# Kernel optimization log

Measured on AMD Instinct MI355X. Metric: run time of the kernel, lower is better.

Reference implementation:

```python
import jax, jax.numpy as jnp
import numpy as np

NUM_HEADS = 4
HEAD_DIM = 32
QUERY_DIM = 256
KEY_DIM = 128
INNER = NUM_HEADS * HEAD_DIM  # 128


def setup_inputs() -> dict:
    key = jax.random.key(0)
    ks = jax.random.split(key, 8)
    B, T, D, H, W = 2, 4, QUERY_DIM, 40, 40
    C, Hm, Wm = KEY_DIM, 40, 40
    query = jax.random.normal(ks[0], (B, T, D, H, W), dtype=jnp.float32)
    k_in = jax.random.normal(ks[1], (B, T, C, Hm, Wm), dtype=jnp.float32)
    v_in = jax.random.normal(ks[2], (B, T, C, Hm, Wm), dtype=jnp.float32)
    # Linear weights stored as (in, out); torch nn.Linear init ~ U(-1/sqrt(in), 1/sqrt(in))
    def lin(k, fan_in, fan_out):
        bound = 1.0 / np.sqrt(fan_in)
        return jax.random.uniform(k, (fan_in, fan_out), minval=-bound, maxval=bound, dtype=jnp.float32)
    Wq = lin(ks[3], QUERY_DIM, INNER)
    Wk = lin(ks[4], KEY_DIM, INNER)
    Wv = lin(ks[5], KEY_DIM, INNER)
    Wo = lin(ks[6], INNER, QUERY_DIM)
    bo = jax.random.uniform(ks[7], (QUERY_DIM,), minval=-1.0 / np.sqrt(INNER), maxval=1.0 / np.sqrt(INNER), dtype=jnp.float32)
    return {"query": query, "key": k_in, "value": v_in,
            "Wq": Wq, "Wk": Wk, "Wv": Wv, "Wo": Wo, "bo": bo}


def reference(query, key, value, Wq, Wk, Wv, Wo, bo):
    B, T, D, H, W = query.shape
    _, _, C, Hm, Wm = key.shape
    scale = HEAD_DIM ** (-0.5)
    # b t d h w -> b t (h w) d
    q = query.reshape(B, T, D, H * W).transpose(0, 1, 3, 2)
    k = key.reshape(B, T, C, Hm * Wm).transpose(0, 1, 3, 2)
    v = value.reshape(B, T, C, Hm * Wm).transpose(0, 1, 3, 2)
    # projections then split heads: b t n (h d) -> b t h n d
    def heads(x):
        Bn, Tn, N, _ = x.shape
        return x.reshape(Bn, Tn, N, NUM_HEADS, HEAD_DIM).transpose(0, 1, 3, 2, 4)
    Q = heads(q @ Wq)
    K = heads(k @ Wk)
    V = heads(v @ Wv)
    scores = jnp.einsum('bthqd,bthkd->bthqk', Q, K) * scale
    probs = jax.nn.softmax(scores, axis=-1)
    out = jnp.einsum('bthqk,bthkd->bthqd', probs, V)
    # b t h n d -> b t n (h d)
    out = out.transpose(0, 1, 3, 2, 4).reshape(B, T, H * W, INNER)
    fused = out @ Wo + bo
    # b t (h w) d -> b t d h w
    return fused.transpose(0, 1, 3, 2).reshape(B, T, D, H, W)
```

## Files before the change

kernel.cpp:

```cpp
#include <hip/hip_runtime.h>

#define NTOK 1600
#define BT_TOTAL 8
#define INNER 128
#define HD 32
#define NH 4
#define QDIM 256

typedef short short8 __attribute__((ext_vector_type(8)));
typedef short short4v __attribute__((ext_vector_type(4)));
typedef float f32x2 __attribute__((ext_vector_type(2)));
typedef float f32x4 __attribute__((ext_vector_type(4)));
typedef float f32x16 __attribute__((ext_vector_type(16)));
typedef unsigned uint2v __attribute__((ext_vector_type(2)));

__device__ inline short f2b(float x) {
  union { float f; unsigned u; } v; v.f = x;
  unsigned r = (v.u + 0x7FFF + ((v.u >> 16) & 1)) >> 16;
  return (short)r;
}
__device__ inline unsigned cvtpk(float a, float b) {
  unsigned r;
  asm("v_cvt_pk_bf16_f32 %0, %1, %2" : "=v"(r) : "v"(a), "v"(b));
  return r;
}
__device__ inline void pswap(unsigned &a, unsigned &b) {
  uint2v r = __builtin_amdgcn_permlane32_swap(a, b, false, false);
  a = r[0]; b = r[1];
}
__device__ inline short8 ldsfrag(const short* p) {
  short4v a = *(const short4v*)p;
  short4v b = *(const short4v*)(p + 4);
  short8 r;
  r[0] = a[0]; r[1] = a[1]; r[2] = a[2]; r[3] = a[3];
  r[4] = b[0]; r[5] = b[1]; r[6] = b[2]; r[7] = b[3];
  return r;
}
__device__ inline short8 mk8(unsigned a, unsigned b, unsigned c, unsigned d) {
  union { unsigned u[4]; short8 v; } t;
  t.u[0] = a; t.u[1] = b; t.u[2] = c; t.u[3] = d;
  return t.v;
}

__global__ __launch_bounds__(256) void proj_fused(
    const float* __restrict__ query, const float* __restrict__ Wq,
    const float* __restrict__ key, const float* __restrict__ Wk,
    const float* __restrict__ value, const float* __restrict__ Wv,
    short* __restrict__ Qbf, short* __restrict__ Kbf,
    short* __restrict__ Vbf) {
  const int n0 = blockIdx.x * 64;
  const int which = blockIdx.y;
  const int bt = blockIdx.z;
  const int t = threadIdx.x;
  const int lane = t & 63, w = t >> 6;
  const int quad = lane >> 4, n16 = lane & 15;

  const float* X; const float* Wt; short* Y; int nchunk; float scl;
  if (which == 0) {
    X = query; Wt = Wq; Y = Qbf; nchunk = 8;
    scl = 0.17677669529663687f * 1.4426950408889634f;
  } else if (which == 1) {
    X = key; Wt = Wk; Y = Kbf; nchunk = 4; scl = 1.0f;
  } else {
    X = value; Wt = Wv; Y = Vbf; nchunk = 4; scl = 1.0f;
  }
  const float* Xb = X + (size_t)bt * (nchunk * 32) * NTOK;

  __shared__ short Xs[64 * 36];
  __shared__ short Ws[128 * 36];

  f32x4 acc[8];
#pragma unroll
  for (int i = 0; i < 8; ++i) acc[i] = (f32x4){0.f, 0.f, 0.f, 0.f};

  const int iw = t & 127, g = t >> 7;

  float xf0[4], xf1[4], wf0[8], wf1[8];
  auto loadX = [&](int cd) {
#pragma unroll
    for (int dp = 0; dp < 4; ++dp) {
      int dl = w * 8 + dp * 2;
      xf0[dp] = Xb[(size_t)(cd + dl) * NTOK + n0 + lane];
      xf1[dp] = Xb[(size_t)(cd + dl + 1) * NTOK + n0 + lane];
    }
  };
  auto loadW = [&](int cd) {
#pragma unroll
    for (int dp = 0; dp < 8; ++dp) {
      int dl = g * 16 + dp * 2;
      wf0[dp] = Wt[(size_t)(cd + dl) * INNER + iw];
      wf1[dp] = Wt[(size_t)(cd + dl + 1) * INNER + iw];
    }
  };
  loadX(0); loadW(0);

  for (int c = 0; c < nchunk; ++c) {
#pragma unroll
    for (int dp = 0; dp < 4; ++dp)
      *(unsigned*)&Xs[lane * 36 + w * 8 + dp * 2] = cvtpk(xf0[dp], xf1[dp]);
#pragma unroll
    for (int dp = 0; dp < 8; ++dp)
      *(unsigned*)&Ws[iw * 36 + g * 16 + dp * 2] = cvtpk(wf0[dp], wf1[dp]);
    __syncthreads();
    if (c + 1 < nchunk) { loadX((c + 1) * 32); loadW((c + 1) * 32); }
    if (which != 2) {
      short8 a[4], b[2];
#pragma unroll
      for (int tg = 0; tg < 4; ++tg)
        a[tg] = ldsfrag(&Xs[(tg * 16 + n16) * 36 + quad * 8]);
#pragma unroll
      for (int cg = 0; cg < 2; ++cg)
        b[cg] = ldsfrag(&Ws[(w * 32 + cg * 16 + n16) * 36 + quad * 8]);
#pragma unroll
      for (int tg = 0; tg < 4; ++tg)
#pragma unroll
        for (int cg = 0; cg < 2; ++cg)
          acc[tg * 2 + cg] = __builtin_amdgcn_mfma_f32_16x16x32_bf16(
              a[tg], b[cg], acc[tg * 2 + cg], 0, 0, 0);
    } else {
      short8 a[2], b[4];
#pragma unroll
      for (int ig = 0; ig < 2; ++ig)
        a[ig] = ldsfrag(&Ws[(w * 32 + ig * 16 + n16) * 36 + quad * 8]);
#pragma unroll
      for (int tg = 0; tg < 4; ++tg)
        b[tg] = ldsfrag(&Xs[(tg * 16 + n16) * 36 + quad * 8]);
#pragma unroll
      for (int ig = 0; ig < 2; ++ig)
#pragma unroll
        for (int tg = 0; tg < 4; ++tg)
          acc[ig * 4 + tg] = __builtin_amdgcn_mfma_f32_16x16x32_bf16(
              a[ig], b[tg], acc[ig * 4 + tg], 0, 0, 0);
    }
    __syncthreads();
  }

  if (which != 2) {
    short* Yb = Y + ((size_t)bt * NH + w) * NTOK * HD;
#pragma unroll
    for (int tg = 0; tg < 4; ++tg)
#pragma unroll
      for (int cg = 0; cg < 2; ++cg) {
        f32x4 a = acc[tg * 2 + cg];
#pragma unroll
        for (int r = 0; r < 4; ++r) {
          int tok = n0 + tg * 16 + quad * 4 + r;
          Yb[(size_t)tok * HD + cg * 16 + n16] = f2b(a[r] * scl);
        }
      }
  } else {
#pragma unroll
    for (int ig = 0; ig < 2; ++ig)
#pragma unroll
      for (int tg = 0; tg < 4; ++tg) {
        f32x4 a = acc[ig * 4 + tg];
#pragma unroll
        for (int r = 0; r < 4; ++r) {
          int irow = w * 32 + ig * 16 + quad * 4 + r;
          Y[((size_t)bt * INNER + irow) * NTOK + n0 + tg * 16 + n16] =
              f2b(a[r]);
        }
      }
  }
}

__global__ __launch_bounds__(256, 3) void attn_mfma(
    const short* __restrict__ Qb, const short* __restrict__ Kb,
    const short* __restrict__ Vb, short* __restrict__ Obf) {
  const int id = blockIdx.x;
  const int qt = id >> 5;
  const int pair = id & 31;
  const int bt = pair >> 2, h = pair & 3;
  const int wave = threadIdx.x >> 6, lane = threadIdx.x & 63;
  const int lh = lane >> 5, q32 = lane & 31;
  const int q0 = qt * 64;
  const size_t btok = ((size_t)bt * NH + h) * NTOK;
  const size_t bd = ((size_t)bt * NH + h) * HD;

  __shared__ float Cb[2][2][17][64];

  const short* QpA = &Qb[(btok + q0 + q32) * HD + lh * 8];
  const short* QpB = QpA + 32 * HD;
  const short8 bqA0 = *(const short8*)(QpA);
  const short8 bqA1 = *(const short8*)(QpA + 16);
  const short8 bqB0 = *(const short8*)(QpB);
  const short8 bqB1 = *(const short8*)(QpB + 16);

  const int kstart = wave * 416 - (wave == 3 ? 32 : 0);
  const int nch = 13 - (wave >> 1);
  const short* Kp = &Kb[(btok + kstart + q32) * HD + lh * 8];
  const short* Vp = &Vb[(bd + q32) * NTOK + kstart + lh * 8];

  const f32x16 zero16 = {0.f, 0.f, 0.f, 0.f, 0.f, 0.f, 0.f, 0.f,
                         0.f, 0.f, 0.f, 0.f, 0.f, 0.f, 0.f, 0.f};
  f32x16 oA = zero16, oB = zero16;
  f32x2 lsA = {0.f, 0.f}, lsB = {0.f, 0.f};

  auto softmax_pack = [&](const f32x16& sv, f32x2& ls2, short8& pb0,
                          short8& pb1) {
    unsigned Pd[8];
#pragma unroll
    for (int g = 0; g < 4; ++g) {
      float e0 = __builtin_amdgcn_exp2f(sv[4 * g + 0]);
      float e1 = __builtin_amdgcn_exp2f(sv[4 * g + 1]);
      float e2 = __builtin_amdgcn_exp2f(sv[4 * g + 2]);
      float e3 = __builtin_amdgcn_exp2f(sv[4 * g + 3]);
      ls2 += (f32x2){e0, e1};
      ls2 += (f32x2){e2, e3};
      Pd[2 * g + 0] = cvtpk(e0, e1);
      Pd[2 * g + 1] = cvtpk(e2, e3);
    }
    pswap(Pd[0], Pd[2]);
    pswap(Pd[1], Pd[3]);
    pswap(Pd[4], Pd[6]);
    pswap(Pd[5], Pd[7]);
    pb0 = mk8(Pd[0], Pd[1], Pd[2], Pd[3]);
    pb1 = mk8(Pd[4], Pd[5], Pd[6], Pd[7]);
  };

  short8 ak0 = *(const short8*)(Kp);
  short8 ak1 = *(const short8*)(Kp + 16);
  short8 av0 = *(const short8*)(Vp);
  short8 av1 = *(const short8*)(Vp + 16);

  for (int i = 0; i < nch; ++i) {
    const size_t kn = (i + 1 < nch) ? (size_t)(i + 1) * 32 : 0;
    short8 nk0 = *(const short8*)(Kp + kn * HD);
    short8 nk1 = *(const short8*)(Kp + kn * HD + 16);
    short8 nv0 = *(const short8*)(Vp + kn);
    short8 nv1 = *(const short8*)(Vp + kn + 16);

    f32x16 sA = __builtin_amdgcn_mfma_f32_32x32x16_bf16(ak0, bqA0, zero16,
                                                        0, 0, 0);
    sA = __builtin_amdgcn_mfma_f32_32x32x16_bf16(ak1, bqA1, sA, 0, 0, 0);
    f32x16 sB = __builtin_amdgcn_mfma_f32_32x32x16_bf16(ak0, bqB0, zero16,
                                                        0, 0, 0);
    sB = __builtin_amdgcn_mfma_f32_32x32x16_bf16(ak1, bqB1, sB, 0, 0, 0);

    short8 pbA0, pbA1, pbB0, pbB1;
    softmax_pack(sA, lsA, pbA0, pbA1);
    softmax_pack(sB, lsB, pbB0, pbB1);

    oA = __builtin_amdgcn_mfma_f32_32x32x16_bf16(av0, pbA0, oA, 0, 0, 0);
    oA = __builtin_amdgcn_mfma_f32_32x32x16_bf16(av1, pbA1, oA, 0, 0, 0);
    oB = __builtin_amdgcn_mfma_f32_32x32x16_bf16(av0, pbB0, oB, 0, 0, 0);
    oB = __builtin_amdgcn_mfma_f32_32x32x16_bf16(av1, pbB1, oB, 0, 0, 0);

    ak0 = nk0; ak1 = nk1; av0 = nv0; av1 = nv1;
  }

  float lsumA = lsA[0] + lsA[1];
  lsumA += __shfl_xor(lsumA, 32);
  float lsumB = lsB[0] + lsB[1];
  lsumB += __shfl_xor(lsumB, 32);

  auto dump = [&](int tl, int sidx, const f32x16& o, float ls) {
#pragma unroll
    for (int r = 0; r < 16; ++r) Cb[tl][sidx][r][lane] = o[r];
    Cb[tl][sidx][16][lane] = ls;
  };
  auto accum = [&](int tl, int sidx, f32x16& o, float& ls) {
#pragma unroll
    for (int r = 0; r < 16; ++r) o[r] += Cb[tl][sidx][r][lane];
    ls += Cb[tl][sidx][16][lane];
  };
  if (wave == 1) { dump(0, 0, oA, lsumA); dump(1, 0, oB, lsumB); }
  if (wave == 3) { dump(0, 1, oA, lsumA); dump(1, 1, oB, lsumB); }
  __syncthreads();
  if (wave == 0) { accum(0, 0, oA, lsumA); accum(1, 0, oB, lsumB); }
  if (wave == 2) { accum(0, 1, oA, lsumA); accum(1, 1, oB, lsumB); }
  __syncthreads();
  if (wave == 2) { dump(0, 0, oA, lsumA); dump(1, 0, oB, lsumB); }
  __syncthreads();
  if (wave == 0) {
    accum(0, 0, oA, lsumA);
    accum(1, 0, oB, lsumB);
    const float invA = 1.f / lsumA;
    short* OpA =
        &Obf[((size_t)bt * NTOK + q0 + q32) * INNER + h * HD + lh * 4];
#pragma unroll
    for (int g = 0; g < 4; ++g) {
      unsigned d0 = cvtpk(oA[4 * g + 0] * invA, oA[4 * g + 1] * invA);
      unsigned d1 = cvtpk(oA[4 * g + 2] * invA, oA[4 * g + 3] * invA);
      *(uint2*)&OpA[8 * g] = make_uint2(d0, d1);
    }
    const float invB = 1.f / lsumB;
    short* OpB =
        &Obf[((size_t)bt * NTOK + q0 + 32 + q32) * INNER + h * HD + lh * 4];
#pragma unroll
    for (int g = 0; g < 4; ++g) {
      unsigned d0 = cvtpk(oB[4 * g + 0] * invB, oB[4 * g + 1] * invB);
      unsigned d1 = cvtpk(oB[4 * g + 2] * invB, oB[4 * g + 3] * invB);
      *(uint2*)&OpB[8 * g] = make_uint2(d0, d1);
    }
  }
}

__global__ __launch_bounds__(256) void oproj_mfma(
    const short* __restrict__ Obf, const float* __restrict__ Wo,
    const float* __restrict__ bo, float* __restrict__ out) {
  const int tok0 = blockIdx.x * 64, d0 = blockIdx.y * 64;
  const int bt = blockIdx.z;
  const int t = threadIdx.x, lane = t & 63, w = t >> 6;
  const int quad = lane >> 4, n16 = lane & 15;
  __shared__ short Wos[64 * 36];
  f32x4 acc[4];
#pragma unroll
  for (int i = 0; i < 4; ++i) acc[i] = (f32x4){0.f, 0.f, 0.f, 0.f};
  const int tok = tok0 + w * 16 + n16;

  float wf0[4], wf1[4];
  short8 bfr;
  auto loadWo = [&](int c) {
#pragma unroll
    for (int dp = 0; dp < 4; ++dp) {
      int il = w * 8 + dp * 2;
      wf0[dp] = Wo[(size_t)(c * 32 + il) * QDIM + d0 + lane];
      wf1[dp] = Wo[(size_t)(c * 32 + il + 1) * QDIM + d0 + lane];
    }
  };
  auto loadB = [&](int c) {
    bfr = *(const short8*)&Obf[((size_t)bt * NTOK + tok) * INNER + c * 32 +
                               quad * 8];
  };
  loadWo(0); loadB(0);

  for (int c = 0; c < 4; ++c) {
#pragma unroll
    for (int dp = 0; dp < 4; ++dp)
      *(unsigned*)&Wos[lane * 36 + w * 8 + dp * 2] = cvtpk(wf0[dp], wf1[dp]);
    __syncthreads();
    short8 b0 = bfr;
    if (c < 3) { loadWo(c + 1); loadB(c + 1); }
#pragma unroll
    for (int ag = 0; ag < 4; ++ag) {
      short8 a = ldsfrag(&Wos[(ag * 16 + n16) * 36 + quad * 8]);
      acc[ag] = __builtin_amdgcn_mfma_f32_16x16x32_bf16(a, b0, acc[ag], 0, 0, 0);
    }
    __syncthreads();
  }

#pragma unroll
  for (int ag = 0; ag < 4; ++ag) {
    f32x4 a = acc[ag];
#pragma unroll
    for (int r = 0; r < 4; ++r) {
      int dout = d0 + ag * 16 + quad * 4 + r;
      out[((size_t)bt * QDIM + dout) * NTOK + tok] = a[r] + bo[dout];
    }
  }
}

extern "C" void kernel_launch(void* const* d_in, const int* in_sizes, int n_in,
                              void* d_out, int out_size, void* d_ws,
                              size_t ws_size, hipStream_t stream) {
  const float* query = (const float*)d_in[0];
  const float* key = (const float*)d_in[1];
  const float* value = (const float*)d_in[2];
  const float* Wq = (const float*)d_in[3];
  const float* Wk = (const float*)d_in[4];
  const float* Wv = (const float*)d_in[5];
  const float* Wo = (const float*)d_in[6];
  const float* bo = (const float*)d_in[7];
  float* out = (float*)d_out;

  const size_t arr = (size_t)BT_TOTAL * INNER * NTOK;
  short* Qbf = (short*)d_ws;
  short* Kbf = Qbf + arr;
  short* Vbf = Kbf + arr;
  short* Obf = Vbf + arr;

  proj_fused<<<dim3(25, 3, BT_TOTAL), 256, 0, stream>>>(
      query, Wq, key, Wk, value, Wv, Qbf, Kbf, Vbf);
  attn_mfma<<<dim3(800), 256, 0, stream>>>(Qbf, Kbf, Vbf, Obf);
  oproj_mfma<<<dim3(25, 4, BT_TOTAL), 256, 0, stream>>>(Obf, Wo, bo, out);
}
```

Baseline: 120.3 us.

## Fuse three kernels into one persistent kernel with grid barriers

Replaces the three separate launches (projection, attention, output projection) with a single persistent kernel of 512 blocks that pull work items from atomic counters and separate the phases with software grid barriers. This is meant to remove launch gaps and tail effects between kernels. The cost is an extra memset, atomic contention, and barrier spin time. Occupancy drops because launch bounds go from 3 to 2 blocks per SM for attention. The design also assumes all 512 blocks are co-resident; if they are not, the grid barrier deadlocks.

Result: slower. 300.9 us (+150.0%).

```diff
diff --git a/kernel.cpp b/kernel.cpp
--- a/kernel.cpp
+++ b/kernel.cpp
@@ -6,6 +6,8 @@
 #define HD 32
 #define NH 4
 #define QDIM 256
+
+#define NBLK 512
 
 typedef short short8 __attribute__((ext_vector_type(8)));
 typedef short short4v __attribute__((ext_vector_type(4)));
@@ -42,15 +44,30 @@
   return t.v;
 }
 
-__global__ __launch_bounds__(256) void proj_fused(
-    const float* __restrict__ query, const float* __restrict__ Wq,
-    const float* __restrict__ key, const float* __restrict__ Wk,
-    const float* __restrict__ value, const float* __restrict__ Wv,
-    short* __restrict__ Qbf, short* __restrict__ Kbf,
-    short* __restrict__ Vbf) {
-  const int n0 = blockIdx.x * 64;
-  const int which = blockIdx.y;
-  const int bt = blockIdx.z;
+__device__ inline void grid_barrier(unsigned* bar, unsigned target) {
+  __syncthreads();
+  if (threadIdx.x == 0) {
+    __threadfence();
+    __hip_atomic_fetch_add(bar, 1u, __ATOMIC_RELAXED,
+                           __HIP_MEMORY_SCOPE_AGENT);
+    while (__hip_atomic_load(bar, __ATOMIC_RELAXED,
+                             __HIP_MEMORY_SCOPE_AGENT) < target) {
+      __builtin_amdgcn_s_sleep(2);
+    }
+    __threadfence();
+  }
+  __syncthreads();
+}
+
+__device__ inline void proj_item(
+    int item, char* smem, const float* __restrict__ query,
+    const float* __restrict__ Wq, const float* __restrict__ key,
+    const float* __restrict__ Wk, const float* __restrict__ value,
+    const float* __restrict__ Wv, short* __restrict__ Qbf,
+    short* __restrict__ Kbf, short* __restrict__ Vbf) {
+  const int n0 = (item % 25) * 64;
+  const int which = (item / 25) % 3;
+  const int bt = item / 75;
   const int t = threadIdx.x;
   const int lane = t & 63, w = t >> 6;
   const int quad = lane >> 4, n16 = lane & 15;
@@ -66,8 +83,8 @@
   }
   const float* Xb = X + (size_t)bt * (nchunk * 32) * NTOK;
 
-  __shared__ short Xs[64 * 36];
-  __shared__ short Ws[128 * 36];
+  short* Xs = (short*)smem;
+  short* Ws = Xs + 64 * 36;
 
   f32x4 acc[8];
 #pragma unroll
@@ -164,12 +181,13 @@
   }
 }
 
-__global__ __launch_bounds__(256, 3) void attn_mfma(
-    const short* __restrict__ Qb, const short* __restrict__ Kb,
-    const short* __restrict__ Vb, short* __restrict__ Obf) {
-  const int id = blockIdx.x;
-  const int qt = id >> 5;
-  const int pair = id & 31;
+__device__ inline void attn_item(int item, char* smem,
+                                 const short* __restrict__ Qb,
+                                 const short* __restrict__ Kb,
+                                 const short* __restrict__ Vb,
+                                 short* __restrict__ Obf) {
+  const int qt = item >> 5;
+  const int pair = item & 31;
   const int bt = pair >> 2, h = pair & 3;
   const int wave = threadIdx.x >> 6, lane = threadIdx.x & 63;
   const int lh = lane >> 5, q32 = lane & 31;
@@ -177,7 +195,7 @@
   const size_t btok = ((size_t)bt * NH + h) * NTOK;
   const size_t bd = ((size_t)bt * NH + h) * HD;
 
-  __shared__ float Cb[2][2][17][64];
+  float (*Cb)[2][17][64] = (float (*)[2][17][64])smem;
 
   const short* QpA = &Qb[(btok + q0 + q32) * HD + lh * 8];
   const short* QpB = QpA + 32 * HD;
@@ -296,14 +314,17 @@
   }
 }
 
-__global__ __launch_bounds__(256) void oproj_mfma(
-    const short* __restrict__ Obf, const float* __restrict__ Wo,
-    const float* __restrict__ bo, float* __restrict__ out) {
-  const int tok0 = blockIdx.x * 64, d0 = blockIdx.y * 64;
-  const int bt = blockIdx.z;
+__device__ inline void oproj_item(int item, char* smem,
+                                  const short* __restrict__ Obf,
+                                  const float* __restrict__ Wo,
+                                  const float* __restrict__ bo,
+                                  float* __restrict__ out) {
+  const int tok0 = (item % 25) * 64;
+  const int d0 = ((item / 25) % 4) * 64;
+  const int bt = item / 100;
   const int t = threadIdx.x, lane = t & 63, w = t >> 6;
   const int quad = lane >> 4, n16 = lane & 15;
-  __shared__ short Wos[64 * 36];
+  short* Wos = (short*)smem;
   f32x4 acc[4];
 #pragma unroll
   for (int i = 0; i < 4; ++i) acc[i] = (f32x4){0.f, 0.f, 0.f, 0.f};
@@ -335,7 +356,8 @@
 #pragma unroll
     for (int ag = 0; ag < 4; ++ag) {
       short8 a = ldsfrag(&Wos[(ag * 16 + n16) * 36 + quad * 8]);
-      acc[ag] = __builtin_amdgcn_mfma_f32_16x16x32_bf16(a, b0, acc[ag], 0, 0, 0);
+      acc[ag] =
+          __builtin_amdgcn_mfma_f32_16x16x32_bf16(a, b0, acc[ag], 0, 0, 0);
     }
     __syncthreads();
   }
@@ -348,6 +370,47 @@
       int dout = d0 + ag * 16 + quad * 4 + r;
       out[((size_t)bt * QDIM + dout) * NTOK + tok] = a[r] + bo[dout];
     }
+  }
+}
+
+__global__ __launch_bounds__(256, 2) void fused_all(
+    const float* __restrict__ query, const float* __restrict__ Wq,
+    const float* __restrict__ key, const float* __restrict__ Wk,
+    const float* __restrict__ value, const float* __restrict__ Wv,
+    const float* __restrict__ Wo, const float* __restrict__ bo,
+    short* __restrict__ Qbf, short* __restrict__ Kbf,
+    short* __restrict__ Vbf, short* __restrict__ Obf,
+    float* __restrict__ out, unsigned* __restrict__ ctrs) {
+  __shared__ __align__(16) char smem[17408];
+  __shared__ int item_s;
+
+  for (;;) {
+    __syncthreads();
+    if (threadIdx.x == 0) item_s = (int)atomicAdd(&ctrs[1], 1u);
+    __syncthreads();
+    const int item = item_s;
+    if (item >= 600) break;
+    proj_item(item, smem, query, Wq, key, Wk, value, Wv, Qbf, Kbf, Vbf);
+  }
+  grid_barrier(&ctrs[0], NBLK);
+
+  for (;;) {
+    __syncthreads();
+    if (threadIdx.x == 0) item_s = (int)atomicAdd(&ctrs[2], 1u);
+    __syncthreads();
+    const int item = item_s;
+    if (item >= 800) break;
+    attn_item(item, smem, Qbf, Kbf, Vbf, Obf);
+  }
+  grid_barrier(&ctrs[0], 2 * NBLK);
+
+  for (;;) {
+    __syncthreads();
+    if (threadIdx.x == 0) item_s = (int)atomicAdd(&ctrs[3], 1u);
+    __syncthreads();
+    const int item = item_s;
+    if (item >= 800) break;
+    oproj_item(item, smem, Obf, Wo, bo, out);
   }
 }
 
@@ -369,9 +432,9 @@
   short* Kbf = Qbf + arr;
   short* Vbf = Kbf + arr;
   short* Obf = Vbf + arr;
-
-  proj_fused<<<dim3(25, 3, BT_TOTAL), 256, 0, stream>>>(
-      query, Wq, key, Wk, value, Wv, Qbf, Kbf, Vbf);
-  attn_mfma<<<dim3(800), 256, 0, stream>>>(Qbf, Kbf, Vbf, Obf);
-  oproj_mfma<<<dim3(25, 4, BT_TOTAL), 256, 0, stream>>>(Obf, Wo, bo, out);
-}
+  unsigned* ctrs = (unsigned*)(Obf + arr);
+
+  hipMemsetAsync(ctrs, 0, 4 * sizeof(unsigned), stream);
+  fused_all<<<dim3(NBLK), dim3(256), 0, stream>>>(
+      query, Wq, key, Wk, value, Wv, Wo, bo, Qbf, Kbf, Vbf, Obf, out, ctrs);
+}
```

## Process five 32-query tiles per attention block to reuse K/V loads

Applied to the files above, without the earlier changes.

Each attention block now handles 160 queries (five 32-row tiles) instead of 64, so every K/V chunk loaded into registers feeds five score/PV MFMA pairs rather than two. The grid shrinks from 800 to 320 blocks and launch bounds drop to 2 blocks per SM to make room for the extra accumulator registers. The cross-wave LDS reduction grows to cover five tiles. The aim is to cut redundant K/V global traffic per query, at the cost of higher register pressure, lower occupancy and fewer blocks to spread across CUs.

Result: slower. 123.1 us (+2.3%).

```diff
diff --git a/kernel.cpp b/kernel.cpp
--- a/kernel.cpp
+++ b/kernel.cpp
@@ -164,27 +164,28 @@
   }
 }
 
-__global__ __launch_bounds__(256, 3) void attn_mfma(
+__global__ __launch_bounds__(256, 2) void attn_mfma(
     const short* __restrict__ Qb, const short* __restrict__ Kb,
     const short* __restrict__ Vb, short* __restrict__ Obf) {
   const int id = blockIdx.x;
-  const int qt = id >> 5;
+  const int qg = id >> 5;
   const int pair = id & 31;
   const int bt = pair >> 2, h = pair & 3;
   const int wave = threadIdx.x >> 6, lane = threadIdx.x & 63;
   const int lh = lane >> 5, q32 = lane & 31;
-  const int q0 = qt * 64;
+  const int q0 = qg * 160;
   const size_t btok = ((size_t)bt * NH + h) * NTOK;
   const size_t bd = ((size_t)bt * NH + h) * HD;
 
-  __shared__ float Cb[2][2][17][64];
-
-  const short* QpA = &Qb[(btok + q0 + q32) * HD + lh * 8];
-  const short* QpB = QpA + 32 * HD;
-  const short8 bqA0 = *(const short8*)(QpA);
-  const short8 bqA1 = *(const short8*)(QpA + 16);
-  const short8 bqB0 = *(const short8*)(QpB);
-  const short8 bqB1 = *(const short8*)(QpB + 16);
+  __shared__ float Cb[5][2][17][64];
+
+  short8 bq0[5], bq1[5];
+#pragma unroll
+  for (int tl = 0; tl < 5; ++tl) {
+    const short* Qp = &Qb[(btok + q0 + tl * 32 + q32) * HD + lh * 8];
+    bq0[tl] = *(const short8*)(Qp);
+    bq1[tl] = *(const short8*)(Qp + 16);
+  }
 
   const int kstart = wave * 416 - (wave == 3 ? 32 : 0);
   const int nch = 13 - (wave >> 1);
@@ -193,8 +194,10 @@
 
   const f32x16 zero16 = {0.f, 0.f, 0.f, 0.f, 0.f, 0.f, 0.f, 0.f,
                          0.f, 0.f, 0.f, 0.f, 0.f, 0.f, 0.f, 0.f};
-  f32x16 oA = zero16, oB = zero16;
-  f32x2 lsA = {0.f, 0.f}, lsB = {0.f, 0.f};
+  f32x16 o[5];
+  f32x2 ls[5];
+#pragma unroll
+  for (int tl = 0; tl < 5; ++tl) { o[tl] = zero16; ls[tl] = (f32x2){0.f, 0.f}; }
 
   auto softmax_pack = [&](const f32x16& sv, f32x2& ls2, short8& pb0,
                           short8& pb1) {
@@ -230,68 +233,73 @@
     short8 nv0 = *(const short8*)(Vp + kn);
     short8 nv1 = *(const short8*)(Vp + kn + 16);
 
-    f32x16 sA = __builtin_amdgcn_mfma_f32_32x32x16_bf16(ak0, bqA0, zero16,
-                                                        0, 0, 0);
-    sA = __builtin_amdgcn_mfma_f32_32x32x16_bf16(ak1, bqA1, sA, 0, 0, 0);
-    f32x16 sB = __builtin_amdgcn_mfma_f32_32x32x16_bf16(ak0, bqB0, zero16,
-                                                        0, 0, 0);
-    sB = __builtin_amdgcn_mfma_f32_32x32x16_bf16(ak1, bqB1, sB, 0, 0, 0);
-
-    short8 pbA0, pbA1, pbB0, pbB1;
-    softmax_pack(sA, lsA, pbA0, pbA1);
-    softmax_pack(sB, lsB, pbB0, pbB1);
-
-    oA = __builtin_amdgcn_mfma_f32_32x32x16_bf16(av0, pbA0, oA, 0, 0, 0);
-    oA = __builtin_amdgcn_mfma_f32_32x32x16_bf16(av1, pbA1, oA, 0, 0, 0);
-    oB = __builtin_amdgcn_mfma_f32_32x32x16_bf16(av0, pbB0, oB, 0, 0, 0);
-    oB = __builtin_amdgcn_mfma_f32_32x32x16_bf16(av1, pbB1, oB, 0, 0, 0);
+#pragma unroll
+    for (int tl = 0; tl < 5; ++tl) {
+      f32x16 s = __builtin_amdgcn_mfma_f32_32x32x16_bf16(ak0, bq0[tl], zero16,
+                                                         0, 0, 0);
+      s = __builtin_amdgcn_mfma_f32_32x32x16_bf16(ak1, bq1[tl], s, 0, 0, 0);
+      short8 pb0, pb1;
+      softmax_pack(s, ls[tl], pb0, pb1);
+      o[tl] = __builtin_amdgcn_mfma_f32_32x32x16_bf16(av0, pb0, o[tl], 0, 0, 0);
+      o[tl] = __builtin_amdgcn_mfma_f32_32x32x16_bf16(av1, pb1, o[tl], 0, 0, 0);
+    }
 
     ak0 = nk0; ak1 = nk1; av0 = nv0; av1 = nv1;
   }
 
-  float lsumA = lsA[0] + lsA[1];
-  lsumA += __shfl_xor(lsumA, 32);
-  float lsumB = lsB[0] + lsB[1];
-  lsumB += __shfl_xor(lsumB, 32);
-
-  auto dump = [&](int tl, int sidx, const f32x16& o, float ls) {
-#pragma unroll
-    for (int r = 0; r < 16; ++r) Cb[tl][sidx][r][lane] = o[r];
-    Cb[tl][sidx][16][lane] = ls;
-  };
-  auto accum = [&](int tl, int sidx, f32x16& o, float& ls) {
-#pragma unroll
-    for (int r = 0; r < 16; ++r) o[r] += Cb[tl][sidx][r][lane];
-    ls += Cb[tl][sidx][16][lane];
-  };
-  if (wave == 1) { dump(0, 0, oA, lsumA); dump(1, 0, oB, lsumB); }
-  if (wave == 3) { dump(0, 1, oA, lsumA); dump(1, 1, oB, lsumB); }
-  __syncthreads();
-  if (wave == 0) { accum(0, 0, oA, lsumA); accum(1, 0, oB, lsumB); }
-  if (wave == 2) { accum(0, 1, oA, lsumA); accum(1, 1, oB, lsumB); }
-  __syncthreads();
-  if (wave == 2) { dump(0, 0, oA, lsumA); dump(1, 0, oB, lsumB); }
+  float lsum[5];
+#pragma unroll
+  for (int tl = 0; tl < 5; ++tl) {
+    lsum[tl] = ls[tl][0] + ls[tl][1];
+    lsum[tl] += __shfl_xor(lsum[tl], 32);
+  }
+
+  auto dump = [&](int tl, int sidx) {
+#pragma unroll
+    for (int r = 0; r < 16; ++r) Cb[tl][sidx][r][lane] = o[tl][r];
+    Cb[tl][sidx][16][lane] = lsum[tl];
+  };
+  auto accum = [&](int tl, int sidx) {
+#pragma unroll
+    for (int r = 0; r < 16; ++r) o[tl][r] += Cb[tl][sidx][r][lane];
+    lsum[tl] += Cb[tl][sidx][16][lane];
+  };
+  if (wave == 1) {
+#pragma unroll
+    for (int tl = 0; tl < 5; ++tl) dump(tl, 0);
+  }
+  if (wave == 3) {
+#pragma unroll
+    for (int tl = 0; tl < 5; ++tl) dump(tl, 1);
+  }
   __syncthreads();
   if (wave == 0) {
-    accum(0, 0, oA, lsumA);
-    accum(1, 0, oB, lsumB);
-    const float invA = 1.f / lsumA;
-    short* OpA =
-        &Obf[((size_t)bt * NTOK + q0 + q32) * INNER + h * HD + lh * 4];
-#pragma unroll
-    for (int g = 0; g < 4; ++g) {
-      unsigned d0 = cvtpk(oA[4 * g + 0] * invA, oA[4 * g + 1] * invA);
-      unsigned d1 = cvtpk(oA[4 * g + 2] * invA, oA[4 * g + 3] * invA);
-      *(uint2*)&OpA[8 * g] = make_uint2(d0, d1);
-    }
-    const float invB = 1.f / lsumB;
-    short* OpB =
-        &Obf[((size_t)bt * NTOK + q0 + 32 + q32) * INNER + h * HD + lh * 4];
-#pragma unroll
-    for (int g = 0; g < 4; ++g) {
-      unsigned d0 = cvtpk(oB[4 * g + 0] * invB, oB[4 * g + 1] * invB);
-      unsigned d1 = cvtpk(oB[4 * g + 2] * invB, oB[4 * g + 3] * invB);
-      *(uint2*)&OpB[8 * g] = make_uint2(d0, d1);
+#pragma unroll
+    for (int tl = 0; tl < 5; ++tl) accum(tl, 0);
+  }
+  if (wave == 2) {
+#pragma unroll
+    for (int tl = 0; tl < 5; ++tl) accum(tl, 1);
+  }
+  __syncthreads();
+  if (wave == 2) {
+#pragma unroll
+    for (int tl = 0; tl < 5; ++tl) dump(tl, 0);
+  }
+  __syncthreads();
+  if (wave == 0) {
+#pragma unroll
+    for (int tl = 0; tl < 5; ++tl) {
+      accum(tl, 0);
+      const float inv = 1.f / lsum[tl];
+      short* Op = &Obf[((size_t)bt * NTOK + q0 + tl * 32 + q32) * INNER +
+                       h * HD + lh * 4];
+#pragma unroll
+      for (int g = 0; g < 4; ++g) {
+        unsigned d0 = cvtpk(o[tl][4 * g + 0] * inv, o[tl][4 * g + 1] * inv);
+        unsigned d1 = cvtpk(o[tl][4 * g + 2] * inv, o[tl][4 * g + 3] * inv);
+        *(uint2*)&Op[8 * g] = make_uint2(d0, d1);
+      }
     }
   }
 }
@@ -372,6 +380,6 @@
 
   proj_fused<<<dim3(25, 3, BT_TOTAL), 256, 0, stream>>>(
       query, Wq, key, Wk, value, Wv, Qbf, Kbf, Vbf);
-  attn_mfma<<<dim3(800), 256, 0, stream>>>(Qbf, Kbf, Vbf, Obf);
+  attn_mfma<<<dim3(320), 256, 0, stream>>>(Qbf, Kbf, Vbf, Obf);
   oproj_mfma<<<dim3(25, 4, BT_TOTAL), 256, 0, stream>>>(Obf, Wo, bo, out);
 }
```
